# Kernel tuning notes

Measured on AMD Instinct MI355X. Metric: run time of the kernel, lower is better.

## Reference

```python
import jax, jax.numpy as jnp
import numpy as np

B = 65536
NUM_INPUTS = 128
H0, H1 = 512, 512
K = 200
MIN_W = 0.001
MIN_H = 0.001
MIN_D = 0.001
EDGE_CONST = float(np.log(np.exp(1.0 - 0.001) - 1.0))  # in-place edge derivative value
LN_EPS = 1e-5


def setup_inputs() -> dict:
    key = jax.random.key(0)
    ks = jax.random.split(key, 10)
    f32 = jnp.float32
    inputs = jax.random.normal(ks[0], (B, NUM_INPUTS), dtype=f32)
    W1 = jax.random.normal(ks[1], (H0, NUM_INPUTS), dtype=f32) / np.sqrt(NUM_INPUTS)
    b1 = jnp.zeros((H0,), f32)
    g1 = jnp.ones((H0,), f32)
    be1 = jnp.zeros((H0,), f32)
    W2 = jax.random.normal(ks[2], (H1, H0), dtype=f32) / np.sqrt(H0)
    b2 = jnp.zeros((H1,), f32)
    g2 = jnp.ones((H1,), f32)
    be2 = jnp.zeros((H1,), f32)
    WV = jax.random.normal(ks[3], (3 * K - 1, H1), dtype=f32) / np.sqrt(H1)
    bV = jnp.zeros((3 * K - 1,), f32)
    Wa = jax.random.normal(ks[4], (1, H1), dtype=f32) / np.sqrt(H1)
    ba = jnp.zeros((1,), f32)
    Wb = jax.random.normal(ks[5], (1, H1), dtype=f32) / np.sqrt(H1)
    bb = jnp.zeros((1,), f32)
    return {"inputs": inputs, "W1": W1, "b1": b1, "g1": g1, "be1": be1,
            "W2": W2, "b2": b2, "g2": g2, "be2": be2,
            "WV": WV, "bV": bV, "Wa": Wa, "ba": ba, "Wb": Wb, "bb": bb}


def _layernorm(x, g, b):
    m = jnp.mean(x, axis=-1, keepdims=True)
    v = jnp.mean(jnp.square(x - m), axis=-1, keepdims=True)
    return (x - m) * jax.lax.rsqrt(v + LN_EPS) * g + b


def _spline_forward(inputs, W1, b1, g1, be1, W2, b2, g2, be2, WV, bV, Wa, ba, Wb, bb):
    x = jax.nn.relu(_layernorm(inputs @ W1.T + b1, g1, be1))
    x = jax.nn.relu(_layernorm(x @ W2.T + b2, g2, be2))
    sp = x @ WV.T + bV                      # [B, 3K-1]
    scale_a = jnp.exp(x @ Wa.T + ba)        # [B, 1]
    scale_b = x @ Wb.T + bb                 # [B, 1]

    Wp = jax.nn.softmax(sp[:, :K], axis=1)
    Hp = jax.nn.softmax(sp[:, K:2 * K], axis=1)
    Dp = sp[:, 2 * K:]                      # [B, K-1]
    Wp = MIN_W + (1.0 - MIN_W * K) * Wp
    Hp = MIN_H + (1.0 - MIN_H * K) * Hp
    Dp = MIN_D + jax.nn.softplus(Dp)
    bsz = inputs.shape[0]
    edge = jnp.full((bsz, 1), EDGE_CONST, dtype=inputs.dtype)
    D = jnp.concatenate([edge, Dp, edge], axis=-1)          # [B, K+1]

    zero = jnp.zeros((bsz, 1), dtype=inputs.dtype)
    cw = jnp.concatenate([zero, jnp.cumsum(Wp, axis=-1)], axis=-1)
    cw = cw.at[:, -1].set(1.0)                              # [B, K+1]
    widths = cw[:, 1:] - cw[:, :-1]                         # [B, K]
    ch = jnp.concatenate([zero, jnp.cumsum(Hp, axis=-1)], axis=-1)
    ch = scale_a * ch + scale_b                             # [B, K+1]
    heights = ch[:, 1:] - ch[:, :-1]                        # [B, K]

    tau = ((jnp.arange(K, dtype=inputs.dtype) + 0.5) / K)   # [K]
    tau = jnp.broadcast_to(tau, (bsz, K))

    # sum(tau >= bins) - 1 == searchsorted(bins, tau, side='right') - 1
    bin_idx = jax.vmap(lambda b, t: jnp.searchsorted(b, t, side='right'))(cw, tau) - 1

    ta = lambda a: jnp.take_along_axis(a, bin_idx, axis=-1)
    in_cw = ta(cw)
    in_w = ta(widths)
    in_ch = ta(ch)
    in_h = ta(heights)
    in_delta = ta(heights / widths)
    d0 = ta(D)
    d1 = ta(D[:, 1:])

    theta = (tau - in_cw) / in_w
    t1mt = theta * (1.0 - theta)
    numer = in_h * (in_delta * jnp.square(theta) + d0 * t1mt)
    denom = in_delta + (d0 + d1 - 2.0 * in_delta) * t1mt
    return in_ch + numer / denom            # [B, K]


def reference(inputs, W1, b1, g1, be1, W2, b2, g2, be2, WV, bV, Wa, ba, Wb, bb):
    return _spline_forward(inputs, W1, b1, g1, be1, W2, b2, g2, be2, WV, bV, Wa, ba, Wb, bb)
```

## Files before the change

kernel.cpp:

```cpp
#include <hip/hip_runtime.h>
#include <stdint.h>

typedef __bf16 bf16;
typedef __bf16 bf16x8 __attribute__((ext_vector_type(8)));
typedef __bf16 bf16x4 __attribute__((ext_vector_type(4)));
typedef float  f32x4  __attribute__((ext_vector_type(4)));
typedef uint32_t u32;

#define BATCH    65536
#define NCAT     640
#define SPSTRIDE 604

__device__ __forceinline__ void async16(const void* g, void* l) {
    __builtin_amdgcn_global_load_lds(
        (const u32 __attribute__((address_space(1)))*)g,
        (u32 __attribute__((address_space(3)))*)l,
        16, 0, 0);
}

__global__ __launch_bounds__(256) void prep_kernel(
    const float* W1, const float* W2, const float* WV,
    const float* bV, const float* Wa, const float* ba,
    const float* Wb, const float* bb, const float* inputs,
    bf16* w1b, bf16* w2b, bf16* wcat, float* bcat, bf16* xin)
{
    int idx = blockIdx.x * 256 + threadIdx.x;
    const int n1 = 512 * 128, n2 = 512 * 512, n3 = NCAT * 512;
    const int n5 = BATCH * 128 / 8;
    if (idx < n5) {
        const float4* src = (const float4*)(inputs + idx * 8);
        float4 v0 = src[0], v1 = src[1];
        bf16x8 h;
        h[0]=(bf16)v0.x; h[1]=(bf16)v0.y; h[2]=(bf16)v0.z; h[3]=(bf16)v0.w;
        h[4]=(bf16)v1.x; h[5]=(bf16)v1.y; h[6]=(bf16)v1.z; h[7]=(bf16)v1.w;
        *(bf16x8*)&xin[idx * 8] = h;
        return;
    }
    idx -= n5;
    if (idx < n1) { w1b[idx] = (bf16)W1[idx]; return; }
    idx -= n1;
    if (idx < n2) { w2b[idx] = (bf16)W2[idx]; return; }
    idx -= n2;
    if (idx < n3) {
        int n = idx >> 9, k = idx & 511;
        float v = 0.f;
        if (n < 599)       v = WV[n * 512 + k];
        else if (n == 599) v = Wa[k];
        else if (n == 600) v = Wb[k];
        wcat[idx] = (bf16)v;
        return;
    }
    idx -= n3;
    if (idx < NCAT) {
        float v = 0.f;
        if (idx < 599)       v = bV[idx];
        else if (idx == 599) v = ba[0];
        else if (idx == 600) v = bb[0];
        bcat[idx] = v;
    }
}

template <int KDIM>
__global__ __launch_bounds__(512, 4) void gemm_ln(
    const bf16* __restrict__ A, const bf16* __restrict__ W,
    const float* __restrict__ bias, const float* __restrict__ gamma,
    const float* __restrict__ beta, bf16* out)
{
    __shared__ __align__(16) char smem[8192 + 65536];
    char* Abase = smem;
    char* Bbase = smem + 8192;

    const int t = threadIdx.x;
    const int lane = t & 63, wid = t >> 6;
    const int wm = wid >> 2, wn = wid & 3;
    const int l16 = lane & 15, g16 = lane >> 4;
    const long row0 = (long)blockIdx.x * 64;
    constexpr int NT = KDIM / 32;

    f32x4 acc[2][8];
#pragma unroll
    for (int a = 0; a < 2; ++a)
#pragma unroll
        for (int b = 0; b < 8; ++b) acc[a][b] = (f32x4){0.f, 0.f, 0.f, 0.f};

    auto stageA = [&](int kt, int bi) {
        if (wid < 4) {
            int row = wid * 16 + (lane >> 2);
            const bf16* src = A + (row0 + row) * (long)KDIM + kt * 32 + (lane & 3) * 8;
            async16(src, Abase + bi * 4096 + wid * 1024);
        }
    };
    auto stageB = [&](int kt, int bi) {
#pragma unroll
        for (int c = 0; c < 4; ++c) {
            int call = wid * 4 + c;
            int row = call * 16 + (lane >> 2);
            const bf16* src = W + (long)row * KDIM + kt * 32 + (lane & 3) * 8;
            async16(src, Bbase + bi * 32768 + call * 1024);
        }
    };

    stageA(0, 0); stageB(0, 0);
    __syncthreads();

    for (int kt = 0; kt < NT; ++kt) {
        const int bi = kt & 1;
        if (kt + 1 < NT) { stageA(kt + 1, bi ^ 1); stageB(kt + 1, bi ^ 1); }
        const bf16* Ab = (const bf16*)(Abase + bi * 4096);
        const bf16* Bb = (const bf16*)(Bbase + bi * 32768);
        bf16x8 af[2];
#pragma unroll
        for (int fm = 0; fm < 2; ++fm)
            af[fm] = *(const bf16x8*)(Ab + (wm * 32 + fm * 16 + l16) * 32 + g16 * 8);
#pragma unroll
        for (int fn = 0; fn < 8; ++fn) {
            bf16x8 bv = *(const bf16x8*)(Bb + (wn * 128 + fn * 16 + l16) * 32 + g16 * 8);
            acc[0][fn] = __builtin_amdgcn_mfma_f32_16x16x32_bf16(af[0], bv, acc[0][fn], 0, 0, 0);
            acc[1][fn] = __builtin_amdgcn_mfma_f32_16x16x32_bf16(af[1], bv, acc[1][fn], 0, 0, 0);
        }
        __syncthreads();
    }

    float* Psum = (float*)Abase;
    float* Psq  = (float*)(Abase + 1024);
    bf16*  stg  = (bf16*)Bbase;
#pragma unroll
    for (int fm = 0; fm < 2; ++fm)
#pragma unroll
        for (int fn = 0; fn < 8; ++fn) {
            float bv = bias[wn * 128 + fn * 16 + l16];
#pragma unroll
            for (int i = 0; i < 4; ++i) acc[fm][fn][i] += bv;
        }
#pragma unroll
    for (int fm = 0; fm < 2; ++fm)
#pragma unroll
        for (int i = 0; i < 4; ++i) {
            float s = 0.f, q = 0.f;
#pragma unroll
            for (int fn = 0; fn < 8; ++fn) { float v = acc[fm][fn][i]; s += v; q += v * v; }
#pragma unroll
            for (int m = 1; m < 16; m <<= 1) { s += __shfl_xor(s, m); q += __shfl_xor(q, m); }
            if (l16 == 0) {
                int lr = wm * 32 + fm * 16 + g16 * 4 + i;
                Psum[lr * 4 + wn] = s; Psq[lr * 4 + wn] = q;
            }
        }
    __syncthreads();
#pragma unroll
    for (int fm = 0; fm < 2; ++fm)
#pragma unroll
        for (int i = 0; i < 4; ++i) {
            int lr = wm * 32 + fm * 16 + g16 * 4 + i;
            float s = Psum[lr * 4 + 0] + Psum[lr * 4 + 1] + Psum[lr * 4 + 2] + Psum[lr * 4 + 3];
            float q = Psq[lr * 4 + 0] + Psq[lr * 4 + 1] + Psq[lr * 4 + 2] + Psq[lr * 4 + 3];
            float mean = s * (1.f / 512.f);
            float var  = q * (1.f / 512.f) - mean * mean;
            float rstd = rsqrtf(var + 1e-5f);
#pragma unroll
            for (int fn = 0; fn < 8; ++fn) {
                int col = wn * 128 + fn * 16 + l16;
                float o = (acc[fm][fn][i] - mean) * rstd * gamma[col] + beta[col];
                stg[lr * 512 + col] = (bf16)fmaxf(o, 0.f);
            }
        }
    __syncthreads();
#pragma unroll
    for (int i = 0; i < 8; ++i) {
        int idx = i * 512 + t;
        *(bf16x8*)&out[(row0 + (idx >> 6)) * 512 + (idx & 63) * 8] =
            *(const bf16x8*)&stg[idx * 8];
    }
}

__global__ __launch_bounds__(512, 4) void gemm_cat(
    const bf16* __restrict__ A, const bf16* __restrict__ W,
    const float* __restrict__ bcat, bf16* __restrict__ sp, float* __restrict__ ab)
{
    __shared__ __align__(16) char smem[8192 + 40960];
    char* Abase = smem;
    char* Bbase = smem + 8192;

    const int t = threadIdx.x;
    const int lane = t & 63, wid = t >> 6;
    const int wm = wid >> 2, wn = wid & 3;
    const int l16 = lane & 15, g16 = lane >> 4;
    const int nh  = blockIdx.x & 1;
    const long row0 = (long)(blockIdx.x >> 1) * 64;

    f32x4 acc[2][5];
#pragma unroll
    for (int a = 0; a < 2; ++a)
#pragma unroll
        for (int b = 0; b < 5; ++b) acc[a][b] = (f32x4){0.f, 0.f, 0.f, 0.f};

    auto stageA = [&](int kt, int bi) {
        if (wid < 4) {
            int row = wid * 16 + (lane >> 2);
            const bf16* src = A + (row0 + row) * 512 + kt * 32 + (lane & 3) * 8;
            async16(src, Abase + bi * 4096 + wid * 1024);
        }
    };
    auto stageB = [&](int kt, int bi) {
#pragma unroll
        for (int c = 0; c < 3; ++c) {
            int call = c * 8 + wid;
            if (call < 20) {
                int row = nh * 320 + call * 16 + (lane >> 2);
                const bf16* src = W + (long)row * 512 + kt * 32 + (lane & 3) * 8;
                async16(src, Bbase + bi * 20480 + call * 1024);
            }
        }
    };

    stageA(0, 0); stageB(0, 0);
    __syncthreads();

    for (int kt = 0; kt < 16; ++kt) {
        const int bi = kt & 1;
        if (kt < 15) { stageA(kt + 1, bi ^ 1); stageB(kt + 1, bi ^ 1); }
        const bf16* Ab = (const bf16*)(Abase + bi * 4096);
        const bf16* Bb = (const bf16*)(Bbase + bi * 20480);
        bf16x8 af[2];
#pragma unroll
        for (int fm = 0; fm < 2; ++fm)
            af[fm] = *(const bf16x8*)(Ab + (wm * 32 + fm * 16 + l16) * 32 + g16 * 8);
#pragma unroll
        for (int fn = 0; fn < 5; ++fn) {
            bf16x8 bv = *(const bf16x8*)(Bb + (wn * 80 + fn * 16 + l16) * 32 + g16 * 8);
            acc[0][fn] = __builtin_amdgcn_mfma_f32_16x16x32_bf16(af[0], bv, acc[0][fn], 0, 0, 0);
            acc[1][fn] = __builtin_amdgcn_mfma_f32_16x16x32_bf16(af[1], bv, acc[1][fn], 0, 0, 0);
        }
        __syncthreads();
    }

    bf16* stg = (bf16*)smem;
#pragma unroll
    for (int fn = 0; fn < 5; ++fn) {
        int lcol = wn * 80 + fn * 16 + l16;
        int col  = nh * 320 + lcol;
        float bv = bcat[col];
#pragma unroll
        for (int fm = 0; fm < 2; ++fm)
#pragma unroll
            for (int i = 0; i < 4; ++i) {
                int r = wm * 32 + fm * 16 + g16 * 4 + i;
                float v = acc[fm][fn][i] + bv;
                stg[r * 320 + lcol] = (bf16)v;
                if (col == 599)      ab[(row0 + r) * 2 + 0] = v;
                else if (col == 600) ab[(row0 + r) * 2 + 1] = v;
            }
    }
    __syncthreads();
    if (nh == 0) {
        for (int c = t; c < 64 * 80; c += 512) {
            int r = c / 80, k = c % 80;
            *(uint64_t*)&sp[(row0 + r) * SPSTRIDE + k * 4] =
                *(const uint64_t*)&stg[r * 320 + k * 4];
        }
    } else {
        for (int c = t; c < 64 * 70; c += 512) {
            int r = c / 70, k = c % 70;
            *(uint64_t*)&sp[(row0 + r) * SPSTRIDE + 320 + k * 4] =
                *(const uint64_t*)&stg[r * 320 + k * 4];
        }
    }
}

__global__ __launch_bounds__(256) void spline_kernel(
    const bf16* __restrict__ sp, const float* __restrict__ ab, float* __restrict__ out)
{
    __shared__ float S[4][816];
    const int t = threadIdx.x;
    const int lane = t & 63, wid = t >> 6;
    const long row = (long)blockIdx.x * 4 + wid;
    const bf16* spr = sp + row * SPSTRIDE;
    const bool act = lane < 50;
    const float EC = 0.53974247f;
    float* cw = &S[wid][0];
    float* ch = &S[wid][204];
    float* dd = &S[wid][408];
    int*   bx = (int*)&S[wid][612];

    const float sa = __expf(ab[row * 2 + 0]);
    const float sb = ab[row * 2 + 1];

    auto rng = [](float x) -> int {
        int v = (int)ceilf(fmaf(200.f, x, -0.5f));
        return v < 0 ? 0 : (v > 200 ? 200 : v);
    };

    float p0, p1, p2, p3;
    {
        float x0, x1, x2v, x3;
        if (act) {
            bf16x4 v = *(const bf16x4*)&spr[4 * lane];
            x0 = (float)v[0]; x1 = (float)v[1]; x2v = (float)v[2]; x3 = (float)v[3];
        } else { x0 = x1 = x2v = x3 = -1e30f; }
        float m = fmaxf(fmaxf(x0, x1), fmaxf(x2v, x3));
#pragma unroll
        for (int d = 1; d < 64; d <<= 1) m = fmaxf(m, __shfl_xor(m, d));
        float e0 = act ? __expf(x0 - m) : 0.f;
        float e1 = act ? __expf(x1 - m) : 0.f;
        float e2 = act ? __expf(x2v - m) : 0.f;
        float e3 = act ? __expf(x3 - m) : 0.f;
        float s = e0 + e1 + e2 + e3;
#pragma unroll
        for (int d = 1; d < 64; d <<= 1) s += __shfl_xor(s, d);
        float inv = 0.8f / s;
        p0 = act ? fmaf(e0, inv, 0.001f) : 0.f;
        p1 = act ? fmaf(e1, inv, 0.001f) : 0.f;
        p2 = act ? fmaf(e2, inv, 0.001f) : 0.f;
        p3 = act ? fmaf(e3, inv, 0.001f) : 0.f;
    }
    float c0 = p0, c1 = c0 + p1, c2 = c1 + p2, c3 = c2 + p3;
    float run = c3, ts = run;
#pragma unroll
    for (int d = 1; d < 64; d <<= 1) { float u = __shfl_up(ts, d); if (lane >= d) ts += u; }
    float excl  = ts - run;
    float nexcl = __shfl_down(excl, 1);
    float cwl0 = excl, cwl1 = excl + c0, cwl2 = excl + c1, cwl3 = excl + c2;

    float hp0, hp1, hp2, hp3;
    {
        float x0, x1, x2v, x3;
        if (act) {
            bf16x4 v = *(const bf16x4*)&spr[200 + 4 * lane];
            x0 = (float)v[0]; x1 = (float)v[1]; x2v = (float)v[2]; x3 = (float)v[3];
        } else { x0 = x1 = x2v = x3 = -1e30f; }
        float m = fmaxf(fmaxf(x0, x1), fmaxf(x2v, x3));
#pragma unroll
        for (int d = 1; d < 64; d <<= 1) m = fmaxf(m, __shfl_xor(m, d));
        float e0 = act ? __expf(x0 - m) : 0.f;
        float e1 = act ? __expf(x1 - m) : 0.f;
        float e2 = act ? __expf(x2v - m) : 0.f;
        float e3 = act ? __expf(x3 - m) : 0.f;
        float s = e0 + e1 + e2 + e3;
#pragma unroll
        for (int d = 1; d < 64; d <<= 1) s += __shfl_xor(s, d);
        float inv = 0.8f / s;
        hp0 = act ? fmaf(e0, inv, 0.001f) : 0.f;
        hp1 = act ? fmaf(e1, inv, 0.001f) : 0.f;
        hp2 = act ? fmaf(e2, inv, 0.001f) : 0.f;
        hp3 = act ? fmaf(e3, inv, 0.001f) : 0.f;
    }
    float hc0 = hp0, hc1 = hc0 + hp1, hc2 = hc1 + hp2, hc3 = hc2 + hp3;
    float hrun = hc3, hts = hrun;
#pragma unroll
    for (int d = 1; d < 64; d <<= 1) { float u = __shfl_up(hts, d); if (lane >= d) hts += u; }
    float hexcl = hts - hrun;
    float ch0 = fmaf(sa, hexcl, sb);
    float ch1 = fmaf(sa, hexcl + hc0, sb);
    float ch2 = fmaf(sa, hexcl + hc1, sb);
    float ch3 = fmaf(sa, hexcl + hc2, sb);

    float dv0, dv1, dv2, dv3;
    {
        float x0 = 0.f, x1 = 0.f, x2v = 0.f, x3 = 0.f;
        if (act) {
            bf16x4 v = *(const bf16x4*)&spr[400 + 4 * lane];
            x0 = (float)v[0]; x1 = (float)v[1]; x2v = (float)v[2]; x3 = (float)v[3];
        }
        auto spls = [](float x) {
            return fmaxf(x, 0.f) + __logf(1.f + __expf(-fabsf(x))) + 0.001f;
        };
        dv0 = spls(x0); dv1 = spls(x1); dv2 = spls(x2v); dv3 = spls(x3);
    }
    if (lane == 49) dv3 = EC;
    float dprev = __shfl_up(dv3, 1);
    if (lane == 0) dprev = EC;

    if (act) {
        *(f32x4*)&cw[4 * lane] = (f32x4){cwl0, cwl1, cwl2, cwl3};
        *(f32x4*)&ch[4 * lane] = (f32x4){ch0, ch1, ch2, ch3};
        *(f32x4*)&dd[4 * lane] = (f32x4){dprev, dv0, dv1, dv2};
    }
    if (lane == 49) {
        cw[200] = 1.0f;
        ch[200] = fmaf(sa, hts, sb);
        dd[200] = EC;
    }

    if (act) {
        int b0 = rng(cwl0), b1 = rng(cwl1), b2 = rng(cwl2), b3 = rng(cwl3);
        int b4 = (lane == 49) ? 200 : rng(nexcl);
        for (int j = b0; j < b1; ++j) bx[j] = 4 * lane;
        for (int j = b1; j < b2; ++j) bx[j] = 4 * lane + 1;
        for (int j = b2; j < b3; ++j) bx[j] = 4 * lane + 2;
        for (int j = b3; j < b4; ++j) bx[j] = 4 * lane + 3;
    }
    asm volatile("s_waitcnt lgkmcnt(0)" ::: "memory");

    if (act) {
        float* orow = out + (size_t)row * 200;
#pragma unroll
        for (int k = 0; k < 4; ++k) {
            int j = lane + 50 * k;
            int b = bx[j];
            float wl = cw[b], wr = cw[b + 1];
            float hl = ch[b], hr = ch[b + 1];
            float d0 = dd[b], d1 = dd[b + 1];
            float tau = ((float)j + 0.5f) * (1.f / 200.f);
            float w = wr - wl, h = hr - hl;
            float invw = 1.f / w;
            float delta = h * invw;
            float th = (tau - wl) * invw;
            float t1 = th * (1.f - th);
            float numer = h * fmaf(delta * th, th, d0 * t1);
            float denom = fmaf(d0 + d1 - 2.f * delta, t1, delta);
            orow[j] = hl + numer / denom;
        }
    }
}

extern "C" void kernel_launch(void* const* d_in, const int* in_sizes, int n_in,
                              void* d_out, int out_size, void* d_ws, size_t ws_size,
                              hipStream_t stream)
{
    const float* inputs = (const float*)d_in[0];
    const float* W1  = (const float*)d_in[1];
    const float* b1  = (const float*)d_in[2];
    const float* g1  = (const float*)d_in[3];
    const float* be1 = (const float*)d_in[4];
    const float* W2  = (const float*)d_in[5];
    const float* b2  = (const float*)d_in[6];
    const float* g2  = (const float*)d_in[7];
    const float* be2 = (const float*)d_in[8];
    const float* WV  = (const float*)d_in[9];
    const float* bV  = (const float*)d_in[10];
    const float* Wa  = (const float*)d_in[11];
    const float* ba  = (const float*)d_in[12];
    const float* Wb  = (const float*)d_in[13];
    const float* bb  = (const float*)d_in[14];
    float* out = (float*)d_out;

    char* ws = (char*)d_ws;
    bf16*  w1b  = (bf16*) (ws + 0);
    bf16*  w2b  = (bf16*) (ws + 131072);
    bf16*  wcat = (bf16*) (ws + 655360);
    float* bcat = (float*)(ws + 1310720);
    float* ab   = (float*)(ws + 1313280);
    bf16*  x    = (bf16*) (ws + 2097152);
    bf16*  spb  = (bf16*) (ws + 69206016);
    bf16*  xin  = (bf16*) (ws + 69206016);

    const int preptot = BATCH * 128 / 8 + 512 * 128 + 512 * 512 + NCAT * 512 + NCAT;
    prep_kernel<<<(preptot + 255) / 256, 256, 0, stream>>>(
        W1, W2, WV, bV, Wa, ba, Wb, bb, inputs, w1b, w2b, wcat, bcat, xin);

    gemm_ln<128><<<BATCH / 64, 512, 0, stream>>>(xin, w1b, b1, g1, be1, x);
    gemm_ln<512><<<BATCH / 64, 512, 0, stream>>>(x,   w2b, b2, g2, be2, x);
    gemm_cat<<<(BATCH / 64) * 2, 512, 0, stream>>>(x, wcat, bcat, spb, ab);
    spline_kernel<<<BATCH / 4, 256, 0, stream>>>(spb, ab, out);
}
```

Baseline: 250.1 us.

## Fuse both MLP layers into one kernel and drop LDS staging of weights

Merges the two GEMM+LayerNorm kernels into one fused_mlp kernel. The first layer's activations stay in swizzled LDS and feed the second GEMM directly, which removes one global round-trip of the 64Kx512 hidden tensor and one launch. All GEMMs now load A and W fragments straight from global memory, relying on cache instead of async LDS double-buffering. gemm_cat now computes all 640 columns per block, which halves its grid and avoids recomputing A tiles. The risks are more uncoalesced global loads, higher register pressure from 20 accumulators, and lower occupancy with the larger LDS footprint.

```diff
diff --git a/kernel.cpp b/kernel.cpp
--- a/kernel.cpp
+++ b/kernel.cpp
@@ -5,18 +5,12 @@
 typedef __bf16 bf16x8 __attribute__((ext_vector_type(8)));
 typedef __bf16 bf16x4 __attribute__((ext_vector_type(4)));
 typedef float  f32x4  __attribute__((ext_vector_type(4)));
-typedef uint32_t u32;
 
 #define BATCH    65536
 #define NCAT     640
 #define SPSTRIDE 604
 
-__device__ __forceinline__ void async16(const void* g, void* l) {
-    __builtin_amdgcn_global_load_lds(
-        (const u32 __attribute__((address_space(1)))*)g,
-        (u32 __attribute__((address_space(3)))*)l,
-        16, 0, 0);
-}
+#define MFMA __builtin_amdgcn_mfma_f32_16x16x32_bf16
 
 __global__ __launch_bounds__(256) void prep_kernel(
     const float* W1, const float* W2, const float* WV,
@@ -60,22 +54,23 @@
     }
 }
 
-template <int KDIM>
-__global__ __launch_bounds__(512, 4) void gemm_ln(
-    const bf16* __restrict__ A, const bf16* __restrict__ W,
-    const float* __restrict__ bias, const float* __restrict__ gamma,
-    const float* __restrict__ beta, bf16* out)
+__global__ __launch_bounds__(512) void fused_mlp(
+    const bf16* __restrict__ xin, const bf16* __restrict__ w1,
+    const float* __restrict__ b1, const float* __restrict__ g1,
+    const float* __restrict__ be1,
+    const bf16* __restrict__ w2,
+    const float* __restrict__ b2, const float* __restrict__ g2,
+    const float* __restrict__ be2,
+    bf16* __restrict__ xout)
 {
-    __shared__ __align__(16) char smem[8192 + 65536];
-    char* Abase = smem;
-    char* Bbase = smem + 8192;
+    __shared__ __align__(16) char X1[65536];
+    __shared__ float Psum[64][4], Psq[64][4];
 
     const int t = threadIdx.x;
     const int lane = t & 63, wid = t >> 6;
     const int wm = wid >> 2, wn = wid & 3;
     const int l16 = lane & 15, g16 = lane >> 4;
     const long row0 = (long)blockIdx.x * 64;
-    constexpr int NT = KDIM / 32;
 
     f32x4 acc[2][8];
 #pragma unroll
@@ -83,52 +78,24 @@
 #pragma unroll
         for (int b = 0; b < 8; ++b) acc[a][b] = (f32x4){0.f, 0.f, 0.f, 0.f};
 
-    auto stageA = [&](int kt, int bi) {
-        if (wid < 4) {
-            int row = wid * 16 + (lane >> 2);
-            const bf16* src = A + (row0 + row) * (long)KDIM + kt * 32 + (lane & 3) * 8;
-            async16(src, Abase + bi * 4096 + wid * 1024);
-        }
-    };
-    auto stageB = [&](int kt, int bi) {
-#pragma unroll
-        for (int c = 0; c < 4; ++c) {
-            int call = wid * 4 + c;
-            int row = call * 16 + (lane >> 2);
-            const bf16* src = W + (long)row * KDIM + kt * 32 + (lane & 3) * 8;
-            async16(src, Bbase + bi * 32768 + call * 1024);
-        }
-    };
-
-    stageA(0, 0); stageB(0, 0);
-    __syncthreads();
-
-    for (int kt = 0; kt < NT; ++kt) {
-        const int bi = kt & 1;
-        if (kt + 1 < NT) { stageA(kt + 1, bi ^ 1); stageB(kt + 1, bi ^ 1); }
-        const bf16* Ab = (const bf16*)(Abase + bi * 4096);
-        const bf16* Bb = (const bf16*)(Bbase + bi * 32768);
-        bf16x8 af[2];
-#pragma unroll
-        for (int fm = 0; fm < 2; ++fm)
-            af[fm] = *(const bf16x8*)(Ab + (wm * 32 + fm * 16 + l16) * 32 + g16 * 8);
+#pragma unroll
+    for (int kt = 0; kt < 4; ++kt) {
+        const int ka = kt * 32 + g16 * 8;
+        bf16x8 af0 = *(const bf16x8*)&xin[(row0 + wm * 32 + l16) * 128 + ka];
+        bf16x8 af1 = *(const bf16x8*)&xin[(row0 + wm * 32 + 16 + l16) * 128 + ka];
 #pragma unroll
         for (int fn = 0; fn < 8; ++fn) {
-            bf16x8 bv = *(const bf16x8*)(Bb + (wn * 128 + fn * 16 + l16) * 32 + g16 * 8);
-            acc[0][fn] = __builtin_amdgcn_mfma_f32_16x16x32_bf16(af[0], bv, acc[0][fn], 0, 0, 0);
-            acc[1][fn] = __builtin_amdgcn_mfma_f32_16x16x32_bf16(af[1], bv, acc[1][fn], 0, 0, 0);
-        }
-        __syncthreads();
-    }
-
-    float* Psum = (float*)Abase;
-    float* Psq  = (float*)(Abase + 1024);
-    bf16*  stg  = (bf16*)Bbase;
+            bf16x8 bv = *(const bf16x8*)&w1[(wn * 128 + fn * 16 + l16) * 128 + ka];
+            acc[0][fn] = MFMA(af0, bv, acc[0][fn], 0, 0, 0);
+            acc[1][fn] = MFMA(af1, bv, acc[1][fn], 0, 0, 0);
+        }
+    }
+
 #pragma unroll
     for (int fm = 0; fm < 2; ++fm)
 #pragma unroll
         for (int fn = 0; fn < 8; ++fn) {
-            float bv = bias[wn * 128 + fn * 16 + l16];
+            float bv = b1[wn * 128 + fn * 16 + l16];
 #pragma unroll
             for (int i = 0; i < 4; ++i) acc[fm][fn][i] += bv;
         }
@@ -143,7 +110,7 @@
             for (int m = 1; m < 16; m <<= 1) { s += __shfl_xor(s, m); q += __shfl_xor(q, m); }
             if (l16 == 0) {
                 int lr = wm * 32 + fm * 16 + g16 * 4 + i;
-                Psum[lr * 4 + wn] = s; Psq[lr * 4 + wn] = q;
+                Psum[lr][wn] = s; Psq[lr][wn] = q;
             }
         }
     __syncthreads();
@@ -152,15 +119,78 @@
 #pragma unroll
         for (int i = 0; i < 4; ++i) {
             int lr = wm * 32 + fm * 16 + g16 * 4 + i;
-            float s = Psum[lr * 4 + 0] + Psum[lr * 4 + 1] + Psum[lr * 4 + 2] + Psum[lr * 4 + 3];
-            float q = Psq[lr * 4 + 0] + Psq[lr * 4 + 1] + Psq[lr * 4 + 2] + Psq[lr * 4 + 3];
+            float s = Psum[lr][0] + Psum[lr][1] + Psum[lr][2] + Psum[lr][3];
+            float q = Psq[lr][0] + Psq[lr][1] + Psq[lr][2] + Psq[lr][3];
             float mean = s * (1.f / 512.f);
             float var  = q * (1.f / 512.f) - mean * mean;
             float rstd = rsqrtf(var + 1e-5f);
 #pragma unroll
             for (int fn = 0; fn < 8; ++fn) {
                 int col = wn * 128 + fn * 16 + l16;
-                float o = (acc[fm][fn][i] - mean) * rstd * gamma[col] + beta[col];
+                float o = (acc[fm][fn][i] - mean) * rstd * g1[col] + be1[col];
+                uint32_t off = (uint32_t)(lr * 1024 + col * 2) ^ (uint32_t)((lr & 7) << 4);
+                *(bf16*)(X1 + off) = (bf16)fmaxf(o, 0.f);
+            }
+        }
+    __syncthreads();
+
+#pragma unroll
+    for (int a = 0; a < 2; ++a)
+#pragma unroll
+        for (int b = 0; b < 8; ++b) acc[a][b] = (f32x4){0.f, 0.f, 0.f, 0.f};
+
+    const int r0 = wm * 32 + l16, r1 = r0 + 16;
+    const uint32_t sw0 = (uint32_t)((r0 & 7) << 4), sw1 = (uint32_t)((r1 & 7) << 4);
+#pragma unroll 4
+    for (int kt = 0; kt < 16; ++kt) {
+        bf16x8 af0 = *(const bf16x8*)(X1 + ((uint32_t)(r0 * 1024 + kt * 64 + g16 * 16) ^ sw0));
+        bf16x8 af1 = *(const bf16x8*)(X1 + ((uint32_t)(r1 * 1024 + kt * 64 + g16 * 16) ^ sw1));
+#pragma unroll
+        for (int fn = 0; fn < 8; ++fn) {
+            bf16x8 bv = *(const bf16x8*)&w2[(wn * 128 + fn * 16 + l16) * 512 + kt * 32 + g16 * 8];
+            acc[0][fn] = MFMA(af0, bv, acc[0][fn], 0, 0, 0);
+            acc[1][fn] = MFMA(af1, bv, acc[1][fn], 0, 0, 0);
+        }
+    }
+
+#pragma unroll
+    for (int fm = 0; fm < 2; ++fm)
+#pragma unroll
+        for (int fn = 0; fn < 8; ++fn) {
+            float bv = b2[wn * 128 + fn * 16 + l16];
+#pragma unroll
+            for (int i = 0; i < 4; ++i) acc[fm][fn][i] += bv;
+        }
+#pragma unroll
+    for (int fm = 0; fm < 2; ++fm)
+#pragma unroll
+        for (int i = 0; i < 4; ++i) {
+            float s = 0.f, q = 0.f;
+#pragma unroll
+            for (int fn = 0; fn < 8; ++fn) { float v = acc[fm][fn][i]; s += v; q += v * v; }
+#pragma unroll
+            for (int m = 1; m < 16; m <<= 1) { s += __shfl_xor(s, m); q += __shfl_xor(q, m); }
+            if (l16 == 0) {
+                int lr = wm * 32 + fm * 16 + g16 * 4 + i;
+                Psum[lr][wn] = s; Psq[lr][wn] = q;
+            }
+        }
+    __syncthreads();
+    bf16* stg = (bf16*)X1;
+#pragma unroll
+    for (int fm = 0; fm < 2; ++fm)
+#pragma unroll
+        for (int i = 0; i < 4; ++i) {
+            int lr = wm * 32 + fm * 16 + g16 * 4 + i;
+            float s = Psum[lr][0] + Psum[lr][1] + Psum[lr][2] + Psum[lr][3];
+            float q = Psq[lr][0] + Psq[lr][1] + Psq[lr][2] + Psq[lr][3];
+            float mean = s * (1.f / 512.f);
+            float var  = q * (1.f / 512.f) - mean * mean;
+            float rstd = rsqrtf(var + 1e-5f);
+#pragma unroll
+            for (int fn = 0; fn < 8; ++fn) {
+                int col = wn * 128 + fn * 16 + l16;
+                float o = (acc[fm][fn][i] - mean) * rstd * g2[col] + be2[col];
                 stg[lr * 512 + col] = (bf16)fmaxf(o, 0.f);
             }
         }
@@ -168,77 +198,45 @@
 #pragma unroll
     for (int i = 0; i < 8; ++i) {
         int idx = i * 512 + t;
-        *(bf16x8*)&out[(row0 + (idx >> 6)) * 512 + (idx & 63) * 8] =
+        *(bf16x8*)&xout[(row0 + (idx >> 6)) * 512 + (idx & 63) * 8] =
             *(const bf16x8*)&stg[idx * 8];
     }
 }
 
-__global__ __launch_bounds__(512, 4) void gemm_cat(
+__global__ __launch_bounds__(512) void gemm_cat(
     const bf16* __restrict__ A, const bf16* __restrict__ W,
     const float* __restrict__ bcat, bf16* __restrict__ sp, float* __restrict__ ab)
 {
-    __shared__ __align__(16) char smem[8192 + 40960];
-    char* Abase = smem;
-    char* Bbase = smem + 8192;
+    __shared__ __align__(16) bf16 stg[64 * SPSTRIDE];
 
     const int t = threadIdx.x;
     const int lane = t & 63, wid = t >> 6;
     const int wm = wid >> 2, wn = wid & 3;
     const int l16 = lane & 15, g16 = lane >> 4;
-    const int nh  = blockIdx.x & 1;
-    const long row0 = (long)(blockIdx.x >> 1) * 64;
-
-    f32x4 acc[2][5];
+    const long row0 = (long)blockIdx.x * 64;
+
+    f32x4 acc[2][10];
 #pragma unroll
     for (int a = 0; a < 2; ++a)
 #pragma unroll
-        for (int b = 0; b < 5; ++b) acc[a][b] = (f32x4){0.f, 0.f, 0.f, 0.f};
-
-    auto stageA = [&](int kt, int bi) {
-        if (wid < 4) {
-            int row = wid * 16 + (lane >> 2);
-            const bf16* src = A + (row0 + row) * 512 + kt * 32 + (lane & 3) * 8;
-            async16(src, Abase + bi * 4096 + wid * 1024);
-        }
-    };
-    auto stageB = [&](int kt, int bi) {
-#pragma unroll
-        for (int c = 0; c < 3; ++c) {
-            int call = c * 8 + wid;
-            if (call < 20) {
-                int row = nh * 320 + call * 16 + (lane >> 2);
-                const bf16* src = W + (long)row * 512 + kt * 32 + (lane & 3) * 8;
-                async16(src, Bbase + bi * 20480 + call * 1024);
-            }
-        }
-    };
-
-    stageA(0, 0); stageB(0, 0);
-    __syncthreads();
-
+        for (int b = 0; b < 10; ++b) acc[a][b] = (f32x4){0.f, 0.f, 0.f, 0.f};
+
+#pragma unroll 4
     for (int kt = 0; kt < 16; ++kt) {
-        const int bi = kt & 1;
-        if (kt < 15) { stageA(kt + 1, bi ^ 1); stageB(kt + 1, bi ^ 1); }
-        const bf16* Ab = (const bf16*)(Abase + bi * 4096);
-        const bf16* Bb = (const bf16*)(Bbase + bi * 20480);
-        bf16x8 af[2];
-#pragma unroll
-        for (int fm = 0; fm < 2; ++fm)
-            af[fm] = *(const bf16x8*)(Ab + (wm * 32 + fm * 16 + l16) * 32 + g16 * 8);
-#pragma unroll
-        for (int fn = 0; fn < 5; ++fn) {
-            bf16x8 bv = *(const bf16x8*)(Bb + (wn * 80 + fn * 16 + l16) * 32 + g16 * 8);
-            acc[0][fn] = __builtin_amdgcn_mfma_f32_16x16x32_bf16(af[0], bv, acc[0][fn], 0, 0, 0);
-            acc[1][fn] = __builtin_amdgcn_mfma_f32_16x16x32_bf16(af[1], bv, acc[1][fn], 0, 0, 0);
-        }
-        __syncthreads();
-    }
-
-    bf16* stg = (bf16*)smem;
-#pragma unroll
-    for (int fn = 0; fn < 5; ++fn) {
-        int lcol = wn * 80 + fn * 16 + l16;
-        int col  = nh * 320 + lcol;
+        const int ka = kt * 32 + g16 * 8;
+        bf16x8 af0 = *(const bf16x8*)&A[(row0 + wm * 32 + l16) * 512 + ka];
+        bf16x8 af1 = *(const bf16x8*)&A[(row0 + wm * 32 + 16 + l16) * 512 + ka];
+#pragma unroll
+        for (int fn = 0; fn < 10; ++fn) {
+            bf16x8 bv = *(const bf16x8*)&W[(wn * 160 + fn * 16 + l16) * 512 + ka];
+            acc[0][fn] = MFMA(af0, bv, acc[0][fn], 0, 0, 0);
+            acc[1][fn] = MFMA(af1, bv, acc[1][fn], 0, 0, 0);
+        }
+    }
+
+#pragma unroll
+    for (int fn = 0; fn < 10; ++fn) {
+        int col = wn * 160 + fn * 16 + l16;
         float bv = bcat[col];
 #pragma unroll
         for (int fm = 0; fm < 2; ++fm)
@@ -246,24 +244,16 @@
             for (int i = 0; i < 4; ++i) {
                 int r = wm * 32 + fm * 16 + g16 * 4 + i;
                 float v = acc[fm][fn][i] + bv;
-                stg[r * 320 + lcol] = (bf16)v;
+                if (col < SPSTRIDE) stg[r * SPSTRIDE + col] = (bf16)v;
                 if (col == 599)      ab[(row0 + r) * 2 + 0] = v;
                 else if (col == 600) ab[(row0 + r) * 2 + 1] = v;
             }
     }
     __syncthreads();
-    if (nh == 0) {
-        for (int c = t; c < 64 * 80; c += 512) {
-            int r = c / 80, k = c % 80;
-            *(uint64_t*)&sp[(row0 + r) * SPSTRIDE + k * 4] =
-                *(const uint64_t*)&stg[r * 320 + k * 4];
-        }
-    } else {
-        for (int c = t; c < 64 * 70; c += 512) {
-            int r = c / 70, k = c % 70;
-            *(uint64_t*)&sp[(row0 + r) * SPSTRIDE + 320 + k * 4] =
-                *(const uint64_t*)&stg[r * 320 + k * 4];
-        }
+    for (int c = t; c < 64 * 151; c += 512) {
+        int r = c / 151, k = c - r * 151;
+        *(uint64_t*)&sp[(row0 + r) * SPSTRIDE + k * 4] =
+            *(const uint64_t*)&stg[r * SPSTRIDE + k * 4];
     }
 }
 
@@ -448,8 +438,8 @@
     prep_kernel<<<(preptot + 255) / 256, 256, 0, stream>>>(
         W1, W2, WV, bV, Wa, ba, Wb, bb, inputs, w1b, w2b, wcat, bcat, xin);
 
-    gemm_ln<128><<<BATCH / 64, 512, 0, stream>>>(xin, w1b, b1, g1, be1, x);
-    gemm_ln<512><<<BATCH / 64, 512, 0, stream>>>(x,   w2b, b2, g2, be2, x);
-    gemm_cat<<<(BATCH / 64) * 2, 512, 0, stream>>>(x, wcat, bcat, spb, ab);
+    fused_mlp<<<BATCH / 64, 512, 0, stream>>>(
+        xin, w1b, b1, g1, be1, w2b, b2, g2, be2, x);
+    gemm_cat<<<BATCH / 64, 512, 0, stream>>>(x, wcat, bcat, spb, ab);
     spline_kernel<<<BATCH / 4, 256, 0, stream>>>(spb, ab, out);
 }
```

After: 447.1 us. +78.8%, slower.
